# Performance work log

Hardware: AMD Instinct MI355X
Metric: run time of the kernel (lower is better)

## Reference

```python
import jax, jax.numpy as jnp
import numpy as np

EMBED = 1280
H = 20
D = 64
MAX_CACHE_LEN = 2048
NEG = -1e30


def setup_inputs() -> dict:
    key = jax.random.key(0)
    ks = jax.random.split(key, 6)
    w = lambda k: jax.random.normal(k, (EMBED, EMBED), dtype=jnp.float32) * 0.02
    return {
        "hidden_states": jax.random.normal(ks[0], (1, 2048, EMBED), dtype=jnp.float32),
        "wq": w(ks[1]), "bq": jnp.zeros((EMBED,), jnp.float32),
        "wk": w(ks[2]),
        "wv": w(ks[3]), "bv": jnp.zeros((EMBED,), jnp.float32),
        "wo": w(ks[4]), "bo": jnp.zeros((EMBED,), jnp.float32),
        "pos_int": 0,
    }


def reference(hidden_states, wq, bq, wk, wv, bv, wo, bo, pos_int):
    B, T, E = hidden_states.shape
    scale = D ** -0.5
    # projections (torch Linear: x @ W^T + b); Whisper k_proj has no bias
    q = (hidden_states @ wq.T + bq).reshape(B, T, H, D).transpose(0, 2, 1, 3)
    k = (hidden_states @ wk.T).reshape(B, T, H, D).transpose(0, 2, 1, 3)
    v = (hidden_states @ wv.T + bv).reshape(B, T, H, D).transpose(0, 2, 1, 3)
    # static KV-cache update (ETKVCache.update): write k,v at [pos:pos+T]
    k_cache = jnp.zeros((B, H, MAX_CACHE_LEN, D), hidden_states.dtype)
    v_cache = jnp.zeros((B, H, MAX_CACHE_LEN, D), hidden_states.dtype)
    k_cache = jax.lax.dynamic_update_slice(k_cache, k, (0, 0, pos_int, 0))
    v_cache = jax.lax.dynamic_update_slice(v_cache, v, (0, 0, pos_int, 0))
    end_pos = pos_int + T
    k_win = k_cache[:, :, :end_pos, :]  # [B,H,S,D]
    v_win = v_cache[:, :, :end_pos, :]
    # SDPA with is_causal=True: torch uses top-left aligned tril(T, S) mask
    scores = jnp.einsum("bhtd,bhsd->bhts", q, k_win) * scale
    mask = jnp.tril(jnp.ones((T, end_pos), dtype=bool))
    scores = jnp.where(mask, scores, NEG)
    attn = jax.nn.softmax(scores, axis=-1)
    out = jnp.einsum("bhts,bhsd->bhtd", attn, v_win)
    out = out.transpose(0, 2, 1, 3).reshape(B, T, H * D)
    return out @ wo.T + bo
```

## Files before the change

### kernel.cpp

```cpp
#include <hip/hip_runtime.h>
#include <hip/hip_bf16.h>

typedef __bf16 bf16;
typedef __bf16 bf16x8 __attribute__((ext_vector_type(8)));
typedef float  f32x4  __attribute__((ext_vector_type(4)));
typedef float  f32x16 __attribute__((ext_vector_type(16)));
typedef unsigned int u32;
typedef u32 u32x4 __attribute__((ext_vector_type(4)));

#define AS1 __attribute__((address_space(1)))
#define AS3 __attribute__((address_space(3)))

#define T_LEN 2048
#define EMB   1280
#define NH    20
#define HD    64

#define NCHUNK_PER_HEAD 40

#define QSCALE 0.18033688011112042f

__device__ __forceinline__ void gl_lds16(const void* gsrc, void* ldst) {
  __builtin_amdgcn_global_load_lds((AS1 void*)const_cast<void*>(gsrc),
                                   (AS3 void*)ldst, 16, 0, 0);
}

__global__ __launch_bounds__(256) void cvt_all(
    const float* __restrict__ hs, const float* __restrict__ wq,
    const float* __restrict__ wk, const float* __restrict__ wv,
    const float* __restrict__ wo, bf16* __restrict__ out) {
  const int HS8 = T_LEN * EMB / 8;
  const int W8  = EMB * EMB / 8;
  int i = blockIdx.x * 256 + threadIdx.x;
  const float* src;
  bf16* dst;
  int off;
  if (i < HS8)              { src = hs; dst = out;                              off = i; }
  else if (i < HS8 + W8)    { src = wq; dst = out + (size_t)T_LEN * EMB;        off = i - HS8; }
  else if (i < HS8 + 2*W8)  { src = wk; dst = out + (size_t)T_LEN*EMB +   (size_t)EMB*EMB; off = i - HS8 - W8; }
  else if (i < HS8 + 3*W8)  { src = wv; dst = out + (size_t)T_LEN*EMB + 2*(size_t)EMB*EMB; off = i - HS8 - 2*W8; }
  else if (i < HS8 + 4*W8)  { src = wo; dst = out + (size_t)T_LEN*EMB + 3*(size_t)EMB*EMB; off = i - HS8 - 3*W8; }
  else return;
  const float4* p4 = (const float4*)src;
  float4 a = p4[2 * off], b = p4[2 * off + 1];
  bf16x8 o;
  o[0] = (bf16)a.x; o[1] = (bf16)a.y; o[2] = (bf16)a.z; o[3] = (bf16)a.w;
  o[4] = (bf16)b.x; o[5] = (bf16)b.y; o[6] = (bf16)b.z; o[7] = (bf16)b.w;
  *(bf16x8*)(dst + (size_t)off * 8) = o;
}

__global__ __launch_bounds__(256, 2) void gemm_qkv(
    const bf16* __restrict__ hsb,
    const bf16* __restrict__ wqb, const bf16* __restrict__ wkb,
    const bf16* __restrict__ wvb,
    const float* __restrict__ bq, const float* __restrict__ bv,
    bf16* __restrict__ Qb, bf16* __restrict__ Kb, bf16* __restrict__ VTb)
{
  constexpr int NK = EMB / 64;
  __shared__ alignas(16) bf16 As[2][128 * 64];
  __shared__ alignas(16) bf16 Bs[2][128 * 64];

  const int g = blockIdx.x & 7, local = blockIdx.x >> 3;
  const int sub = local / 10;
  const int bn = local % 10;
  const int bm = g * 2 + (sub & 1);
  const int mode = sub >> 1;
  const bf16* B = (mode == 0) ? wqb : (mode == 1) ? wkb : wvb;
  const int rowbase = bm * 128;

  const int lane = threadIdx.x & 63;
  const int w = threadIdx.x >> 6;
  const int wr = w >> 1, wc = w & 1;
  const int g4 = lane >> 4, c = lane & 15;

  const f32x4 z4 = {0.f, 0.f, 0.f, 0.f};
  f32x4 acc[4][4];
  #pragma unroll
  for (int i = 0; i < 4; ++i)
    #pragma unroll
    for (int j = 0; j < 4; ++j) acc[i][j] = z4;

  auto STAGE = [&](int b, int kt) {
    #pragma unroll
    for (int i = 0; i < 4; ++i) {
      const int call = w * 4 + i;
      const int slot = call * 1024 + lane * 16;
      const int row = slot >> 7;
      const int scb = (slot & 127) ^ ((row & 7) << 4);
      gl_lds16((const char*)hsb + (size_t)(rowbase + row) * (EMB * 2) + kt * 128 + scb,
               (char*)As[b] + call * 1024);
    }
    #pragma unroll
    for (int i = 0; i < 4; ++i) {
      const int call = w * 4 + i;
      const int slot = call * 1024 + lane * 16;
      const int row = slot >> 7;
      const int scb = (slot & 127) ^ ((row & 7) << 4);
      gl_lds16((const char*)B + (size_t)(bn * 128 + row) * (EMB * 2) + kt * 128 + scb,
               (char*)Bs[b] + call * 1024);
    }
  };

  STAGE(0, 0);
  for (int kt = 0; kt < NK; ++kt) {
    const int cur = kt & 1;
    STAGE(cur ^ 1, kt + 1 < NK ? kt + 1 : kt);
    asm volatile("s_waitcnt vmcnt(8)" ::: "memory");
    __builtin_amdgcn_s_barrier();
    asm volatile("" ::: "memory");
    const bf16* Asc = As[cur];
    const bf16* Bsc = Bs[cur];
    #pragma unroll
    for (int kc = 0; kc < 2; ++kc) {
      bf16x8 af[4], bfr[4];
      #pragma unroll
      for (int mt = 0; mt < 4; ++mt) {
        const int row = wr * 64 + mt * 16 + c;
        const int off = row * 128 + ((kc * 64 + g4 * 16) ^ ((row & 7) << 4));
        af[mt] = *(const bf16x8*)((const char*)Asc + off);
      }
      #pragma unroll
      for (int nt = 0; nt < 4; ++nt) {
        const int row = wc * 64 + nt * 16 + c;
        const int off = row * 128 + ((kc * 64 + g4 * 16) ^ ((row & 7) << 4));
        bfr[nt] = *(const bf16x8*)((const char*)Bsc + off);
      }
      #pragma unroll
      for (int mt = 0; mt < 4; ++mt)
        #pragma unroll
        for (int nt = 0; nt < 4; ++nt)
          acc[mt][nt] = __builtin_amdgcn_mfma_f32_16x16x32_bf16(af[mt], bfr[nt],
                                                                acc[mt][nt], 0, 0, 0);
    }
    asm volatile("" ::: "memory");
    __builtin_amdgcn_s_barrier();
  }

  #pragma unroll
  for (int mt = 0; mt < 4; ++mt) {
    const int t0 = rowbase + wr * 64 + mt * 16 + g4 * 4;
    #pragma unroll
    for (int nt = 0; nt < 4; ++nt) {
      const int n = bn * 128 + wc * 64 + nt * 16 + c;
      const int h = n >> 6, d = n & 63;
      #pragma unroll
      for (int r = 0; r < 4; ++r) {
        const int t = t0 + r;
        float v = acc[mt][nt][r];
        if (mode == 0) {
          v = (v + bq[n]) * QSCALE;
          Qb[((size_t)h * T_LEN + t) * HD + d] = (bf16)v;
        } else if (mode == 1) {
          Kb[((size_t)h * T_LEN + t) * HD + d] = (bf16)v;
        } else {
          v += bv[n];
          VTb[((size_t)h * HD + d) * T_LEN + t] = (bf16)v;
        }
      }
    }
  }
}

__global__ __launch_bounds__(128, 2) void gemm_o(
    const bf16* __restrict__ aob, const bf16* __restrict__ wob,
    const float* __restrict__ bo, float* __restrict__ Out)
{
  constexpr int NK = EMB / 64;
  __shared__ alignas(16) bf16 As[2][64 * 64];
  __shared__ alignas(16) bf16 Bs[2][64 * 64];

  const int g = blockIdx.x & 7, local = blockIdx.x >> 3;
  const int bm = g * 4 + local / 20;
  const int bn = local % 20;
  const int rowbase = bm * 64;

  const int lane = threadIdx.x & 63;
  const int w = threadIdx.x >> 6;
  const int g4 = lane >> 4, c = lane & 15;

  const f32x4 z4 = {0.f, 0.f, 0.f, 0.f};
  f32x4 acc[2][4];
  #pragma unroll
  for (int i = 0; i < 2; ++i)
    #pragma unroll
    for (int j = 0; j < 4; ++j) acc[i][j] = z4;

  auto STAGE = [&](int b, int kt) {
    #pragma unroll
    for (int i = 0; i < 4; ++i) {
      const int call = w * 4 + i;
      const int slot = call * 1024 + lane * 16;
      const int row = slot >> 7;
      const int scb = (slot & 127) ^ ((row & 7) << 4);
      gl_lds16((const char*)aob + (size_t)(rowbase + row) * (EMB * 2) + kt * 128 + scb,
               (char*)As[b] + call * 1024);
    }
    #pragma unroll
    for (int i = 0; i < 4; ++i) {
      const int call = w * 4 + i;
      const int slot = call * 1024 + lane * 16;
      const int row = slot >> 7;
      const int scb = (slot & 127) ^ ((row & 7) << 4);
      gl_lds16((const char*)wob + (size_t)(bn * 64 + row) * (EMB * 2) + kt * 128 + scb,
               (char*)Bs[b] + call * 1024);
    }
  };

  STAGE(0, 0);
  for (int kt = 0; kt < NK; ++kt) {
    const int cur = kt & 1;
    STAGE(cur ^ 1, kt + 1 < NK ? kt + 1 : kt);
    asm volatile("s_waitcnt vmcnt(8)" ::: "memory");
    __builtin_amdgcn_s_barrier();
    asm volatile("" ::: "memory");
    const bf16* Asc = As[cur];
    const bf16* Bsc = Bs[cur];
    #pragma unroll
    for (int kc = 0; kc < 2; ++kc) {
      bf16x8 af[2], bfr[4];
      #pragma unroll
      for (int mt = 0; mt < 2; ++mt) {
        const int row = w * 32 + mt * 16 + c;
        const int off = row * 128 + ((kc * 64 + g4 * 16) ^ ((row & 7) << 4));
        af[mt] = *(const bf16x8*)((const char*)Asc + off);
      }
      #pragma unroll
      for (int nt = 0; nt < 4; ++nt) {
        const int row = nt * 16 + c;
        const int off = row * 128 + ((kc * 64 + g4 * 16) ^ ((row & 7) << 4));
        bfr[nt] = *(const bf16x8*)((const char*)Bsc + off);
      }
      #pragma unroll
      for (int mt = 0; mt < 2; ++mt)
        #pragma unroll
        for (int nt = 0; nt < 4; ++nt)
          acc[mt][nt] = __builtin_amdgcn_mfma_f32_16x16x32_bf16(af[mt], bfr[nt],
                                                                acc[mt][nt], 0, 0, 0);
    }
    asm volatile("" ::: "memory");
    __builtin_amdgcn_s_barrier();
  }

  #pragma unroll
  for (int mt = 0; mt < 2; ++mt) {
    const int t0 = rowbase + w * 32 + mt * 16 + g4 * 4;
    #pragma unroll
    for (int nt = 0; nt < 4; ++nt) {
      const int n = bn * 64 + nt * 16 + c;
      #pragma unroll
      for (int r = 0; r < 4; ++r)
        Out[(size_t)(t0 + r) * EMB + n] = acc[mt][nt][r] + bo[n];
    }
  }
}

__global__ __launch_bounds__(256, 4) void attn_fwd(
    const bf16* __restrict__ Qb, const bf16* __restrict__ Kb,
    const bf16* __restrict__ VTb, bf16* __restrict__ AOb,
    bf16* __restrict__ Pob, float* __restrict__ Pml)
{
  __shared__ alignas(16) bf16 kbuf[2][64 * 64];
  __shared__ alignas(16) bf16 vbuf[2][64 * 64];

  const int bid = blockIdx.x;
  const int h   = bid / NCHUNK_PER_HEAD;
  const int idx = (NCHUNK_PER_HEAD - 1) - bid % NCHUNK_PER_HEAD;
  int qb, ch, nch;
  if (idx < 4)       { qb = idx;                ch = 0;      nch = 1; }
  else if (idx < 12) { int t = idx - 4;  qb = 4 + (t >> 1);  ch = t & 1;  nch = 2; }
  else if (idx < 24) { int t = idx - 12; qb = 8 + t / 3;     ch = t % 3;  nch = 3; }
  else               { int t = idx - 24; qb = 12 + (t >> 2); ch = t & 3;  nch = 4; }
  const int nj = 2 * qb + 2;
  const int j0 = ch * 8;
  const int j1 = (j0 + 8 < nj) ? j0 + 8 : nj;

  const int lane = threadIdx.x & 63;
  const int w  = threadIdx.x >> 6;
  const int l31 = lane & 31;
  const int hi  = lane >> 5;
  const int q0 = qb * 128;
  const int q  = q0 + w * 32 + l31;

  bf16x8 qf[4];
  {
    const char* qrow = (const char*)Qb + ((size_t)h * T_LEN + q) * (HD * 2);
    #pragma unroll
    for (int ds = 0; ds < 4; ++ds)
      qf[ds] = *(const bf16x8*)(qrow + ds * 32 + hi * 16);
  }

  f32x16 oacc[2];
  #pragma unroll
  for (int r = 0; r < 16; ++r) { oacc[0][r] = 0.f; oacc[1][r] = 0.f; }
  float m_r = -1e30f, ls = 0.f;

  auto STAGE = [&](int b, int j) {
    const int s0 = j * 64;
    #pragma unroll
    for (int i = 0; i < 2; ++i) {
      const int call = w * 2 + i;
      const int slot = call * 1024 + lane * 16;
      const int row = slot >> 7;
      const int col = (slot & 127) ^ ((row & 7) << 4);
      gl_lds16((const char*)Kb + ((size_t)h * T_LEN + s0 + row) * (HD * 2) + col,
               (char*)kbuf[b] + call * 1024);
      gl_lds16((const char*)VTb + (((size_t)h * HD + row) * T_LEN + s0) * 2 + col,
               (char*)vbuf[b] + call * 1024);
    }
  };

  auto AFRAG = [&](const bf16* buf, int rblk, int colb) -> bf16x8 {
    const int row = rblk * 32 + l31;
    const int off = row * 128 + ((colb + hi * 16) ^ ((row & 7) << 4));
    return *(const bf16x8*)((const char*)buf + off);
  };

  STAGE(0, j0);
  int cur = 0;
  for (int j = j0; j < j1; ++j) {
    STAGE(cur ^ 1, j + 1 < j1 ? j + 1 : j);
    asm volatile("s_waitcnt vmcnt(4)" ::: "memory");
    __builtin_amdgcn_s_barrier();
    asm volatile("" ::: "memory");

    f32x16 sv[2];
    #pragma unroll
    for (int r = 0; r < 16; ++r) { sv[0][r] = 0.f; sv[1][r] = 0.f; }
    #pragma unroll
    for (int ds = 0; ds < 4; ++ds) {
      #pragma unroll
      for (int sb = 0; sb < 2; ++sb) {
        bf16x8 kf = AFRAG(kbuf[cur], sb, ds * 32);
        sv[sb] = __builtin_amdgcn_mfma_f32_32x32x16_bf16(kf, qf[ds], sv[sb], 0, 0, 0);
      }
    }

    if (j >= 2 * qb) {
      const int s0 = j * 64;
      #pragma unroll
      for (int sb = 0; sb < 2; ++sb)
        #pragma unroll
        for (int r = 0; r < 16; ++r) {
          const int s = s0 + sb * 32 + (r & 3) + 8 * (r >> 2) + 4 * hi;
          if (s > q) sv[sb][r] = -1e30f;
        }
    }

    float pm = sv[0][0];
    #pragma unroll
    for (int r = 1; r < 16; ++r) pm = fmaxf(pm, sv[0][r]);
    #pragma unroll
    for (int r = 0; r < 16; ++r) pm = fmaxf(pm, sv[1][r]);
    pm = fmaxf(pm, __shfl_xor(pm, 32));
    const float mn = fmaxf(m_r, pm);
    const float sc = __builtin_amdgcn_exp2f(m_r - mn);
    m_r = mn;
    float ps = 0.f;
    #pragma unroll
    for (int sb = 0; sb < 2; ++sb)
      #pragma unroll
      for (int r = 0; r < 16; ++r) {
        const float p = __builtin_amdgcn_exp2f(sv[sb][r] - mn);
        sv[sb][r] = p;
        ps += p;
      }
    ls = ls * sc + ps;
    oacc[0] *= sc;
    oacc[1] *= sc;

    u32 wds[16], xds[16];
    #pragma unroll
    for (int i = 0; i < 8; ++i) {
      asm("v_cvt_pk_bf16_f32 %0, %1, %2" : "=v"(wds[i])     : "v"(sv[0][2*i]), "v"(sv[0][2*i+1]));
      asm("v_cvt_pk_bf16_f32 %0, %1, %2" : "=v"(wds[8 + i]) : "v"(sv[1][2*i]), "v"(sv[1][2*i+1]));
    }
    #pragma unroll
    for (int i = 0; i < 16; ++i) xds[i] = (u32)__shfl_xor((int)wds[i], 32);

    #pragma unroll
    for (int ks = 0; ks < 4; ++ks) {
      const int o = (ks >> 1) * 8 + (ks & 1) * 4;
      u32x4 fw;
      fw.x = hi ? xds[o + 2] : wds[o];
      fw.y = hi ? xds[o + 3] : wds[o + 1];
      fw.z = hi ? wds[o + 2] : xds[o];
      fw.w = hi ? wds[o + 3] : xds[o + 1];
      bf16x8 pf = __builtin_bit_cast(bf16x8, fw);
      #pragma unroll
      for (int db = 0; db < 2; ++db) {
        bf16x8 vf = AFRAG(vbuf[cur], db, ks * 32);
        oacc[db] = __builtin_amdgcn_mfma_f32_32x32x16_bf16(vf, pf, oacc[db], 0, 0, 0);
      }
    }

    asm volatile("" ::: "memory");
    __builtin_amdgcn_s_barrier();
    cur ^= 1;
  }

  const float lt = ls + __shfl_xor(ls, 32);

  if (nch == 1) {
    const float inv = 1.f / lt;
    char* orow = (char*)AOb + ((size_t)q * EMB + h * HD) * 2;
    #pragma unroll
    for (int db = 0; db < 2; ++db)
      #pragma unroll
      for (int i = 0; i < 8; ++i) {
        const float lo = oacc[db][2 * i] * inv;
        const float hv = oacc[db][2 * i + 1] * inv;
        u32 pk;
        asm("v_cvt_pk_bf16_f32 %0, %1, %2" : "=v"(pk) : "v"(lo), "v"(hv));
        const int d = db * 32 + 8 * (i >> 1) + 2 * (i & 1) + 4 * hi;
        *(u32*)(orow + d * 2) = pk;
      }
  } else {
    const int pi = h * NCHUNK_PER_HEAD + idx;
    const int rowloc = w * 32 + l31;
    bf16* pr = Pob + ((size_t)pi * 128 + rowloc) * 64;
    #pragma unroll
    for (int db = 0; db < 2; ++db)
      #pragma unroll
      for (int i = 0; i < 8; ++i) {
        u32 pk;
        asm("v_cvt_pk_bf16_f32 %0, %1, %2" : "=v"(pk) : "v"(oacc[db][2*i]), "v"(oacc[db][2*i+1]));
        const int d = db * 32 + 8 * (i >> 1) + 2 * (i & 1) + 4 * hi;
        *(u32*)((char*)pr + d * 2) = pk;
      }
    if (hi == 0) {
      float* ml = Pml + ((size_t)pi * 128 + rowloc) * 2;
      ml[0] = m_r;
      ml[1] = lt;
    }
  }
}

__global__ __launch_bounds__(256) void attn_combine(
    const bf16* __restrict__ Pob, const float* __restrict__ Pml,
    bf16* __restrict__ AOb)
{
  const int gw = (blockIdx.x * 256 + threadIdx.x) >> 6;
  const int lane = threadIdx.x & 63;
  const int h  = gw / 1536;
  const int rr = gw % 1536;
  const int qb = 4 + rr / 128;
  const int rl = rr % 128;
  const int nch   = (qb < 8) ? 2 : (qb < 12) ? 3 : 4;
  const int ibase = (qb < 8) ? 4 + 2 * (qb - 4)
                   : (qb < 12) ? 12 + 3 * (qb - 8)
                   : 24 + 4 * (qb - 12);
  const int pi0 = h * NCHUNK_PER_HEAD + ibase;

  float mv[4], lv[4];
  float m = -1e30f;
  for (int c2 = 0; c2 < nch; ++c2) {
    const float* ml = Pml + ((size_t)(pi0 + c2) * 128 + rl) * 2;
    mv[c2] = ml[0];
    lv[c2] = ml[1];
    m = fmaxf(m, mv[c2]);
  }
  float acc = 0.f, l = 0.f;
  for (int c2 = 0; c2 < nch; ++c2) {
    const float sc = __builtin_amdgcn_exp2f(mv[c2] - m);
    const float ov = (float)Pob[((size_t)(pi0 + c2) * 128 + rl) * 64 + lane];
    acc += sc * ov;
    l   += sc * lv[c2];
  }
  const int qrow = qb * 128 + rl;
  AOb[(size_t)qrow * EMB + h * HD + lane] = (bf16)(acc / l);
}

extern "C" void kernel_launch(void* const* d_in, const int* in_sizes, int n_in,
                              void* d_out, int out_size, void* d_ws, size_t ws_size,
                              hipStream_t stream) {
  const float* hs = (const float*)d_in[0];
  const float* wq = (const float*)d_in[1];
  const float* bq = (const float*)d_in[2];
  const float* wk = (const float*)d_in[3];
  const float* wv = (const float*)d_in[4];
  const float* bv = (const float*)d_in[5];
  const float* wo = (const float*)d_in[6];
  const float* bo = (const float*)d_in[7];

  bf16* p = (bf16*)d_ws;
  bf16* hsb = p;  p += (size_t)T_LEN * EMB;
  bf16* wqb = p;  p += (size_t)EMB * EMB;
  bf16* wkb = p;  p += (size_t)EMB * EMB;
  bf16* wvb = p;  p += (size_t)EMB * EMB;
  bf16* wob = p;  p += (size_t)EMB * EMB;
  bf16* Qb  = p;  p += (size_t)NH * T_LEN * HD;
  bf16* Kb  = p;  p += (size_t)NH * T_LEN * HD;
  bf16* VTb = p;  p += (size_t)NH * HD * T_LEN;
  bf16* AOb = p;  p += (size_t)T_LEN * EMB;

  bf16*  Pob = (bf16*)d_ws;
  float* Pml = (float*)((char*)d_ws + (size_t)NH * NCHUNK_PER_HEAD * 128 * 64 * 2);

  const int TOT8 = T_LEN * EMB / 8 + 4 * (EMB * EMB / 8);
  cvt_all<<<(TOT8 + 255) / 256, 256, 0, stream>>>(hs, wq, wk, wv, wo, (bf16*)d_ws);

  gemm_qkv<<<dim3(480), 256, 0, stream>>>(hsb, wqb, wkb, wvb, bq, bv, Qb, Kb, VTb);
  attn_fwd<<<dim3(NH * NCHUNK_PER_HEAD), 256, 0, stream>>>(Qb, Kb, VTb, AOb, Pob, Pml);
  attn_combine<<<dim3(NH * 1536 / 4), 256, 0, stream>>>(Pob, Pml, AOb);
  gemm_o<<<dim3(640), 128, 0, stream>>>(AOb, wob, bo, (float*)d_out);
}
```

Measured before the change: 113.9 us.

## Split attention KV into finer chunks, interleave heads, skip redundant rescale

Attention work is split into KV chunks of 4 blocks instead of 8, giving 72 chunks per head (1440 blocks) instead of 40. Block-to-head mapping is interleaved so heads are spread across CUs. The kernel gets a higher occupancy hint, and the online-softmax rescale is skipped when no lane's running max changes. Partial outputs now live in their own workspace region rather than aliasing the converted inputs. The aim is better load balance and fewer idle CUs, at the cost of more partial writes and a larger combine pass.

```diff
diff --git a/kernel.cpp b/kernel.cpp
--- a/kernel.cpp
+++ b/kernel.cpp
@@ -16,13 +16,18 @@
 #define NH    20
 #define HD    64
 
-#define NCHUNK_PER_HEAD 40
+#define CHUNKS_PER_HEAD 72
 
 #define QSCALE 0.18033688011112042f
 
 __device__ __forceinline__ void gl_lds16(const void* gsrc, void* ldst) {
   __builtin_amdgcn_global_load_lds((AS1 void*)const_cast<void*>(gsrc),
                                    (AS3 void*)ldst, 16, 0, 0);
+}
+
+__device__ __forceinline__ int chunk_base(int q) {
+  const int m = q >> 1;
+  return (q & 1) ? (m + 1) * (m + 1) : m * (m + 1);
 }
 
 __global__ __launch_bounds__(256) void cvt_all(
@@ -254,7 +259,7 @@
   }
 }
 
-__global__ __launch_bounds__(256, 4) void attn_fwd(
+__global__ __launch_bounds__(256, 5) void attn_fwd(
     const bf16* __restrict__ Qb, const bf16* __restrict__ Kb,
     const bf16* __restrict__ VTb, bf16* __restrict__ AOb,
     bf16* __restrict__ Pob, float* __restrict__ Pml)
@@ -263,16 +268,17 @@
   __shared__ alignas(16) bf16 vbuf[2][64 * 64];
 
   const int bid = blockIdx.x;
-  const int h   = bid / NCHUNK_PER_HEAD;
-  const int idx = (NCHUNK_PER_HEAD - 1) - bid % NCHUNK_PER_HEAD;
-  int qb, ch, nch;
-  if (idx < 4)       { qb = idx;                ch = 0;      nch = 1; }
-  else if (idx < 12) { int t = idx - 4;  qb = 4 + (t >> 1);  ch = t & 1;  nch = 2; }
-  else if (idx < 24) { int t = idx - 12; qb = 8 + t / 3;     ch = t % 3;  nch = 3; }
-  else               { int t = idx - 24; qb = 12 + (t >> 2); ch = t & 3;  nch = 4; }
-  const int nj = 2 * qb + 2;
-  const int j0 = ch * 8;
-  const int j1 = (j0 + 8 < nj) ? j0 + 8 : nj;
+  const int h   = bid % NH;
+  const int idx = bid / NH;
+  int qb = 0;
+  #pragma unroll
+  for (int q2 = 1; q2 < 16; ++q2)
+    if (idx >= chunk_base(q2)) qb = q2;
+  const int ch  = idx - chunk_base(qb);
+  const int nch = (qb + 2) >> 1;
+  const int nj  = 2 * qb + 2;
+  const int j0  = ch * 4;
+  const int j1  = (j0 + 4 < nj) ? j0 + 4 : nj;
 
   const int lane = threadIdx.x & 63;
   const int w  = threadIdx.x >> 6;
@@ -352,21 +358,24 @@
     #pragma unroll
     for (int r = 0; r < 16; ++r) pm = fmaxf(pm, sv[1][r]);
     pm = fmaxf(pm, __shfl_xor(pm, 32));
-    const float mn = fmaxf(m_r, pm);
-    const float sc = __builtin_amdgcn_exp2f(m_r - mn);
-    m_r = mn;
+    if (!__all(pm <= m_r)) {
+      const float mn = fmaxf(m_r, pm);
+      const float sc = __builtin_amdgcn_exp2f(m_r - mn);
+      m_r = mn;
+      ls *= sc;
+      oacc[0] *= sc;
+      oacc[1] *= sc;
+    }
     float ps = 0.f;
     #pragma unroll
     for (int sb = 0; sb < 2; ++sb)
       #pragma unroll
       for (int r = 0; r < 16; ++r) {
-        const float p = __builtin_amdgcn_exp2f(sv[sb][r] - mn);
+        const float p = __builtin_amdgcn_exp2f(sv[sb][r] - m_r);
         sv[sb][r] = p;
         ps += p;
       }
-    ls = ls * sc + ps;
-    oacc[0] *= sc;
-    oacc[1] *= sc;
+    ls += ps;
 
     u32 wds[16], xds[16];
     #pragma unroll
@@ -415,7 +424,7 @@
         *(u32*)(orow + d * 2) = pk;
       }
   } else {
-    const int pi = h * NCHUNK_PER_HEAD + idx;
+    const int pi = h * CHUNKS_PER_HEAD + idx;
     const int rowloc = w * 32 + l31;
     bf16* pr = Pob + ((size_t)pi * 128 + rowloc) * 64;
     #pragma unroll
@@ -441,30 +450,23 @@
 {
   const int gw = (blockIdx.x * 256 + threadIdx.x) >> 6;
   const int lane = threadIdx.x & 63;
-  const int h  = gw / 1536;
-  const int rr = gw % 1536;
-  const int qb = 4 + rr / 128;
+  const int h  = gw / 1792;
+  const int rr = gw % 1792;
+  const int qb = 2 + rr / 128;
   const int rl = rr % 128;
-  const int nch   = (qb < 8) ? 2 : (qb < 12) ? 3 : 4;
-  const int ibase = (qb < 8) ? 4 + 2 * (qb - 4)
-                   : (qb < 12) ? 12 + 3 * (qb - 8)
-                   : 24 + 4 * (qb - 12);
-  const int pi0 = h * NCHUNK_PER_HEAD + ibase;
-
-  float mv[4], lv[4];
+  const int nch = (qb + 2) >> 1;
+  const int pi0 = h * CHUNKS_PER_HEAD + chunk_base(qb);
+
   float m = -1e30f;
+  for (int c2 = 0; c2 < nch; ++c2)
+    m = fmaxf(m, Pml[((size_t)(pi0 + c2) * 128 + rl) * 2]);
+
+  float acc = 0.f, l = 0.f;
   for (int c2 = 0; c2 < nch; ++c2) {
     const float* ml = Pml + ((size_t)(pi0 + c2) * 128 + rl) * 2;
-    mv[c2] = ml[0];
-    lv[c2] = ml[1];
-    m = fmaxf(m, mv[c2]);
-  }
-  float acc = 0.f, l = 0.f;
-  for (int c2 = 0; c2 < nch; ++c2) {
-    const float sc = __builtin_amdgcn_exp2f(mv[c2] - m);
-    const float ov = (float)Pob[((size_t)(pi0 + c2) * 128 + rl) * 64 + lane];
-    acc += sc * ov;
-    l   += sc * lv[c2];
+    const float sc = __builtin_amdgcn_exp2f(ml[0] - m);
+    acc += sc * (float)Pob[((size_t)(pi0 + c2) * 128 + rl) * 64 + lane];
+    l   += sc * ml[1];
   }
   const int qrow = qb * 128 + rl;
   AOb[(size_t)qrow * EMB + h * HD + lane] = (bf16)(acc / l);
@@ -492,15 +494,14 @@
   bf16* Kb  = p;  p += (size_t)NH * T_LEN * HD;
   bf16* VTb = p;  p += (size_t)NH * HD * T_LEN;
   bf16* AOb = p;  p += (size_t)T_LEN * EMB;
-
-  bf16*  Pob = (bf16*)d_ws;
-  float* Pml = (float*)((char*)d_ws + (size_t)NH * NCHUNK_PER_HEAD * 128 * 64 * 2);
+  bf16* Pob = p;  p += (size_t)NH * CHUNKS_PER_HEAD * 128 * 64;
+  float* Pml = (float*)p;
 
   const int TOT8 = T_LEN * EMB / 8 + 4 * (EMB * EMB / 8);
   cvt_all<<<(TOT8 + 255) / 256, 256, 0, stream>>>(hs, wq, wk, wv, wo, (bf16*)d_ws);
 
   gemm_qkv<<<dim3(480), 256, 0, stream>>>(hsb, wqb, wkb, wvb, bq, bv, Qb, Kb, VTb);
-  attn_fwd<<<dim3(NH * NCHUNK_PER_HEAD), 256, 0, stream>>>(Qb, Kb, VTb, AOb, Pob, Pml);
-  attn_combine<<<dim3(NH * 1536 / 4), 256, 0, stream>>>(Pob, Pml, AOb);
+  attn_fwd<<<dim3(NH * CHUNKS_PER_HEAD), 256, 0, stream>>>(Qb, Kb, VTb, AOb, Pob, Pml);
+  attn_combine<<<dim3(NH * 1792 / 4), 256, 0, stream>>>(Pob, Pml, AOb);
   gemm_o<<<dim3(640), 128, 0, stream>>>(AOb, wob, bo, (float*)d_out);
 }
```

After: 141.1 us. 1.24x slower.
